# Performance work log

Hardware: AMD Instinct MI355X
Metric: run time of the kernel (lower is better)

Reference implementation:

```python
import jax, jax.numpy as jnp
import numpy as np

B, T, I, H = 64, 128, 1024, 4096
NNZ_IH, NNZ_HH = 262144, 1048576
LN_EPS = 1e-5


def spmm(rows, cols, vals, x, n_out):
    # y[r, b] = sum_{e: rows[e]==r} vals[e] * x[cols[e], b]
    return jax.ops.segment_sum(vals[:, None] * x[cols], rows, num_segments=n_out)


def setup_inputs() -> dict:
    key = jax.random.key(0)
    ks = jax.random.split(key, 8)
    x = jax.random.normal(ks[0], (B, T, I), dtype=jnp.float32)
    ih_rows = jax.random.randint(ks[1], (NNZ_IH,), 0, H, dtype=jnp.int32)
    ih_cols = jax.random.randint(ks[2], (NNZ_IH,), 0, I, dtype=jnp.int32)
    ih_vals = jax.random.normal(ks[3], (NNZ_IH,), dtype=jnp.float32) * 0.02
    hh_rows = jax.random.randint(ks[4], (NNZ_HH,), 0, H, dtype=jnp.int32)
    hh_cols = jax.random.randint(ks[5], (NNZ_HH,), 0, H, dtype=jnp.int32)
    hh_vals = jax.random.normal(ks[6], (NNZ_HH,), dtype=jnp.float32) * 0.02
    return {
        "x": x,
        "ih_rows": ih_rows, "ih_cols": ih_cols, "ih_vals": ih_vals,
        "hh_rows": hh_rows, "hh_cols": hh_cols, "hh_vals": hh_vals,
        "b_ih": jnp.zeros((H,), jnp.float32),
        "b_hh": jnp.zeros((H,), jnp.float32),
        "ln_gamma": jnp.ones((H,), jnp.float32),
        "ln_beta": jnp.zeros((H,), jnp.float32),
    }


def reference(x, ih_rows, ih_cols, ih_vals, hh_rows, hh_cols, hh_vals,
              b_ih, b_hh, ln_gamma, ln_beta):
    # batch_first input (B, T, I) -> (T, I, B), matching torch permute(1, 2, 0)
    xt = jnp.transpose(x, (1, 2, 0))

    def step(h, x_t):
        pre = (spmm(ih_rows, ih_cols, ih_vals, x_t, H) + b_ih[:, None]
               + spmm(hh_rows, hh_cols, hh_vals, h, H) + b_hh[:, None])
        h_act = jnp.tanh(pre)  # (H, B)
        # layernorm over hidden dim (applied on h.t() in torch)
        mu = jnp.mean(h_act, axis=0, keepdims=True)
        var = jnp.mean((h_act - mu) ** 2, axis=0, keepdims=True)
        h_norm = (h_act - mu) * jax.lax.rsqrt(var + LN_EPS)
        h_new = h_norm * ln_gamma[:, None] + ln_beta[:, None]
        return h_new, h_new

    h0 = jnp.zeros((H, B), jnp.float32)
    h_last, out = jax.lax.scan(step, h0, xt)  # out: (T, H, B)
    out = jnp.transpose(out, (2, 0, 1))       # (B, T, H) batch_first
    h_last = h_last.T                         # (B, H)
    return out, h_last
```

## Files before the change

kernel.cpp:

```cpp
#include <hip/hip_runtime.h>
#include <hip/hip_bf16.h>
#include <cstdint>

#define TT 128
#define BB 64
#define II 1024
#define HD 4096
#define N_IH 262144
#define N_HH 1048576
#define LN_EPS 1e-5f
#define NREP 16

typedef unsigned int u32;
typedef unsigned short u16;
typedef float f32x2 __attribute__((ext_vector_type(2)));

__device__ __forceinline__ u32 f2bf_bits(float f) {
  u32 u = __float_as_uint(f);
  return (u + 0x7FFFu + ((u >> 16) & 1u)) >> 16;
}


__global__ void k_hist(const int* __restrict__ rows, int n, int* __restrict__ hist) {
  int e = blockIdx.x * 256 + threadIdx.x;
  if (e < n) atomicAdd(&hist[rows[e] * 64 + (blockIdx.x & 63)], 1);
}

__global__ __launch_bounds__(256) void k_rowtot(const int* __restrict__ hist, int* __restrict__ rowtot) {
  int w = threadIdx.x >> 6, lane = threadIdx.x & 63;
  int row = blockIdx.x * 4 + w;
  int c = hist[row * 64 + lane];
#pragma unroll
  for (int d = 1; d < 64; d <<= 1) c += __shfl_xor(c, d);
  if (lane == 0) rowtot[row] = (c + 7) & ~7;
}

__global__ void k_scan2(const int* __restrict__ rowtot, int* __restrict__ rp) {
  int lane = threadIdx.x;
  int total = 0;
  for (int j = 0; j < 64; ++j) total += rowtot[lane * 64 + j];
  int x = total;
  for (int d = 1; d < 64; d <<= 1) {
    int y = __shfl_up(x, d, 64);
    if (lane >= d) x += y;
  }
  int run = x - total;
  for (int j = 0; j < 64; ++j) {
    int idx = lane * 64 + j;
    rp[idx] = run;
    run += rowtot[idx];
  }
  if (lane == 63) rp[HD] = run;
}

__global__ __launch_bounds__(256) void k_repbase(const int* __restrict__ hist, const int* __restrict__ rp,
                                                 int* __restrict__ cur) {
  int w = threadIdx.x >> 6, lane = threadIdx.x & 63;
  int row = blockIdx.x * 4 + w;
  int c = hist[row * 64 + lane];
  int x = c;
#pragma unroll
  for (int d = 1; d < 64; d <<= 1) {
    int y = __shfl_up(x, d, 64);
    if (lane >= d) x += y;
  }
  cur[row * 64 + lane] = rp[row] + (x - c);
}

__global__ void k_scatter(const int* __restrict__ rows, const int* __restrict__ cols,
                          const float* __restrict__ vals, int n,
                          int* __restrict__ cur, u32* __restrict__ meta,
                          const float* __restrict__ gamma, const float* __restrict__ beta,
                          float* __restrict__ rvg_rep, float* __restrict__ rvb_rep, int fold) {
  int e = blockIdx.x * 256 + threadIdx.x;
  if (e >= n) return;
  int rep = blockIdx.x & 63;
  int r = rows[e], c = cols[e];
  float v = vals[e];
  float vg = v;
  if (fold) {
    vg = v * gamma[c];
    atomicAdd(&rvg_rep[r * 64 + rep], vg);
    atomicAdd(&rvb_rep[r * 64 + rep], v * beta[c]);
  }
  u32 word = (f2bf_bits(vg) << 16) | (u32)c;
  int pos = atomicAdd(&cur[r * 64 + rep], 1);
  meta[pos] = word;
}

__global__ __launch_bounds__(256) void k_rvred(const float* __restrict__ rvg_rep,
                                               const float* __restrict__ rvb_rep,
                                               float* __restrict__ rowvg, float* __restrict__ rowvb) {
  int w = threadIdx.x >> 6, lane = threadIdx.x & 63;
  int row = blockIdx.x * 4 + w;
  float a = rvg_rep[row * 64 + lane];
  float b = rvb_rep[row * 64 + lane];
#pragma unroll
  for (int d = 1; d < 64; d <<= 1) { a += __shfl_xor(a, d); b += __shfl_xor(b, d); }
  if (lane == 0) { rowvg[row] = a; rowvb[row] = b; }
}

__global__ __launch_bounds__(256) void k_xt(const float* __restrict__ x, u16* __restrict__ xt) {
  __shared__ u16 tile[64][66];
  int t = blockIdx.x >> 4, i0 = (blockIdx.x & 15) << 6;
  int w = threadIdx.x >> 6, lane = threadIdx.x & 63;
#pragma unroll
  for (int k = 0; k < 16; ++k) {
    int b = w * 16 + k;
    float v = x[((size_t)b * TT + t) * II + i0 + lane];
    tile[b][lane] = (u16)f2bf_bits(v);
  }
  __syncthreads();
#pragma unroll
  for (int k = 0; k < 16; ++k) {
    int i = w * 16 + k;
    xt[((size_t)t * II + i0 + i) * BB + lane] = tile[lane][i];
  }
}


__device__ __forceinline__ uint4 gld(const char* base, u32 m) {
  return *(const uint4*)(base + ((int)(m & 0xFFFFu) << 7));
}

__device__ __forceinline__ void consume(u32 m, uint4 g, f32x2 acc[4]) {
  float vgf = __uint_as_float(m & 0xFFFF0000u);
  f32x2 vg2 = {vgf, vgf};
  f32x2 p0 = {__uint_as_float(g.x << 16), __uint_as_float(g.x & 0xFFFF0000u)};
  f32x2 p1 = {__uint_as_float(g.y << 16), __uint_as_float(g.y & 0xFFFF0000u)};
  f32x2 p2 = {__uint_as_float(g.z << 16), __uint_as_float(g.z & 0xFFFF0000u)};
  f32x2 p3 = {__uint_as_float(g.w << 16), __uint_as_float(g.w & 0xFFFF0000u)};
  acc[0] += vg2 * p0;
  acc[1] += vg2 * p1;
  acc[2] += vg2 * p2;
  acc[3] += vg2 * p3;
}

__device__ __forceinline__ void gather6(const u32* __restrict__ mp, int n,
                                        const char* __restrict__ base, f32x2 acc[4]) {
  if (n <= 0) return;
  u32 m0 = mp[0], m1 = mp[8], m2 = mp[16], m3 = mp[24], m4 = mp[32], m5 = mp[40];
  uint4 g0 = gld(base, m0), g1 = gld(base, m1), g2 = gld(base, m2),
        g3 = gld(base, m3), g4 = gld(base, m4);
#pragma unroll 6
  for (int it = 0; it < n; ++it) {
    u32 m6 = mp[(it + 6) * 8];
    uint4 g5 = gld(base, m5);
    consume(m0, g0, acc);
    m0 = m1; m1 = m2; m2 = m3; m3 = m4; m4 = m5; m5 = m6;
    g0 = g1; g1 = g2; g2 = g3; g3 = g4; g4 = g5;
  }
}

__global__ __launch_bounds__(256, 8) void k_step(
    const u32* __restrict__ meta_ih, const int* __restrict__ rp_ih,
    const u32* __restrict__ meta_hh, const int* __restrict__ rp_hh,
    const u16* __restrict__ xt_t, const u16* __restrict__ Aprev,
    u16* __restrict__ Acur,
    const float* __restrict__ st_prev, float* __restrict__ st_cur,
    const float* __restrict__ b_ih, const float* __restrict__ b_hh,
    const float* __restrict__ rowvg, const float* __restrict__ rowvb, int first) {
  __shared__ float s_mu[64], s_rs[64], s_sum[64], s_sq[64];
  __shared__ float epil[4][2][64];
  int tid = threadIdx.x;
  int w = tid >> 6, lane = tid & 63;
  if (tid < 64) { s_sum[tid] = 0.f; s_sq[tid] = 0.f; }
  if (!first && tid >= 64 && tid < 128) {
    int b = tid - 64;
    float s = 0.f, q = 0.f;
#pragma unroll
    for (int r2 = 0; r2 < NREP; ++r2) {
      s += st_prev[r2 * 64 + b];
      q += st_prev[NREP * 64 + r2 * 64 + b];
    }
    float mu = s * (1.0f / HD);
    float var = q * (1.0f / HD) - mu * mu;
    s_mu[b] = mu;
    s_rs[b] = rsqrtf(var + LN_EPS);
  }

  int row = blockIdx.x * 2 + (w >> 1);
  int half = w & 1;
  int grp = lane >> 3;
  int l = lane & 7;

  f32x2 acc[4] = {{0,0},{0,0},{0,0},{0,0}};
  {
    int s0 = rp_ih[row];
    int n = (rp_ih[row + 1] - s0) >> 3;
    int nA = (n + 1) >> 1;
    int nn = half ? (n - nA) : nA;
    int sb = s0 + (half ? nA * 8 : 0);
    gather6(meta_ih + sb + grp, nn, (const char*)xt_t + l * 16, acc);
  }
#pragma unroll
  for (int j = 0; j < 4; ++j) {
#pragma unroll
    for (int d = 8; d < 64; d <<= 1) {
      acc[j].x += __shfl_xor(acc[j].x, d);
      acc[j].y += __shfl_xor(acc[j].y, d);
    }
  }
  if (lane < 8) {
#pragma unroll
    for (int j = 0; j < 4; ++j) {
      epil[w][0][lane * 8 + 2 * j] = acc[j].x;
      epil[w][0][lane * 8 + 2 * j + 1] = acc[j].y;
    }
  }

#pragma unroll
  for (int j = 0; j < 4; ++j) { acc[j].x = 0.f; acc[j].y = 0.f; }
  if (!first) {
    int s0 = rp_hh[row];
    int n = (rp_hh[row + 1] - s0) >> 3;
    int nA = (n + 1) >> 1;
    int nn = half ? (n - nA) : nA;
    int sb = s0 + (half ? nA * 8 : 0);
    gather6(meta_hh + sb + grp, nn, (const char*)Aprev + l * 16, acc);
  }
#pragma unroll
  for (int j = 0; j < 4; ++j) {
#pragma unroll
    for (int d = 8; d < 64; d <<= 1) {
      acc[j].x += __shfl_xor(acc[j].x, d);
      acc[j].y += __shfl_xor(acc[j].y, d);
    }
  }
  if (lane < 8) {
#pragma unroll
    for (int j = 0; j < 4; ++j) {
      epil[w][1][lane * 8 + 2 * j] = acc[j].x;
      epil[w][1][lane * 8 + 2 * j + 1] = acc[j].y;
    }
  }

  __syncthreads();
  if (tid < 128) {
    int ridx = tid >> 6;
    int b = tid & 63;
    int row_e = blockIdx.x * 2 + ridx;
    float S_ih = epil[ridx * 2][0][b] + epil[ridx * 2 + 1][0][b];
    float bih = b_ih[row_e], bhh = b_hh[row_e];
    float pre;
    if (first) {
      pre = S_ih + bih + bhh;
    } else {
      float S_hh = epil[ridx * 2][1][b] + epil[ridx * 2 + 1][1][b];
      pre = S_ih + s_rs[b] * (S_hh - s_mu[b] * rowvg[row_e]) + (bih + bhh + rowvb[row_e]);
    }
    float h = 1.0f - 2.0f / (__expf(2.0f * pre) + 1.0f);
    Acur[(size_t)row_e * BB + b] = (u16)f2bf_bits(h);
    atomicAdd(&s_sum[b], h);
    atomicAdd(&s_sq[b], h * h);
  }
  __syncthreads();
  if (tid < 64) {
    int rep = blockIdx.x & (NREP - 1);
    atomicAdd(&st_cur[rep * 64 + tid], s_sum[tid]);
    atomicAdd(&st_cur[NREP * 64 + rep * 64 + tid], s_sq[tid]);
  }
}


__global__ __launch_bounds__(256) void k_out(const u16* __restrict__ A,
                                             const float* __restrict__ stats,
                                             const float* __restrict__ gamma,
                                             const float* __restrict__ beta,
                                             float* __restrict__ out) {
  __shared__ float s_mu[64], s_rs[64];
  __shared__ float tile[64][65];
  int t = blockIdx.x >> 6, r0 = (blockIdx.x & 63) << 6;
  int tid = threadIdx.x, w = tid >> 6, lane = tid & 63;
  const float* st = stats + (size_t)t * (2 * NREP * 64);
  if (tid < 64) {
    float s = 0.f, q = 0.f;
#pragma unroll
    for (int r2 = 0; r2 < NREP; ++r2) {
      s += st[r2 * 64 + tid];
      q += st[NREP * 64 + r2 * 64 + tid];
    }
    float mu = s * (1.0f / HD);
    float var = q * (1.0f / HD) - mu * mu;
    s_mu[tid] = mu;
    s_rs[tid] = rsqrtf(var + LN_EPS);
  }
  __syncthreads();
#pragma unroll
  for (int k = 0; k < 16; ++k) {
    int r = r0 + w * 16 + k;
    float a = __uint_as_float(((u32)A[((size_t)t * HD + r) * BB + lane]) << 16);
    float hn = (a - s_mu[lane]) * s_rs[lane] * gamma[r] + beta[r];
    tile[w * 16 + k][lane] = hn;
  }
  __syncthreads();
#pragma unroll
  for (int k = 0; k < 16; ++k) {
    int b = w * 16 + k;
    float v = tile[lane][b];
    out[((size_t)b * TT + t) * HD + r0 + lane] = v;
    if (t == TT - 1) out[(size_t)BB * TT * HD + (size_t)b * HD + r0 + lane] = v;
  }
}


extern "C" void kernel_launch(void* const* d_in, const int* in_sizes, int n_in,
                              void* d_out, int out_size, void* d_ws, size_t ws_size,
                              hipStream_t stream) {
  const float* x = (const float*)d_in[0];
  const int* ih_rows = (const int*)d_in[1];
  const int* ih_cols = (const int*)d_in[2];
  const float* ih_vals = (const float*)d_in[3];
  const int* hh_rows = (const int*)d_in[4];
  const int* hh_cols = (const int*)d_in[5];
  const float* hh_vals = (const float*)d_in[6];
  const float* b_ih = (const float*)d_in[7];
  const float* b_hh = (const float*)d_in[8];
  const float* gamma = (const float*)d_in[9];
  const float* beta = (const float*)d_in[10];

  char* ws = (char*)d_ws;
  u16* xt = (u16*)(ws + 0);
  u16* A = (u16*)(ws + 16777216);
  u32* meta_ih = (u32*)(ws + 83886080);
  u32* meta_hh = (u32*)(ws + 85065984);
  float* stats = (float*)(ws + 89391616);
  float* rowvg = (float*)(ws + 90440192);
  float* rowvb = (float*)(ws + 90456576);
  int* rp_ih = (int*)(ws + 90472960);
  int* rp_hh = (int*)(ws + 90489600);

  char* scr = ws + 50331648;
  int* hist_ih = (int*)(scr + 0);
  int* hist_hh = (int*)(scr + 1048576);
  int* cur_ih = (int*)(scr + 2097152);
  int* cur_hh = (int*)(scr + 3145728);
  float* rvg_rep = (float*)(scr + 4194304);
  float* rvb_rep = (float*)(scr + 5242880);
  int* rowtot_ih = (int*)(scr + 6291456);
  int* rowtot_hh = (int*)(scr + 6307840);

  hipMemsetAsync(scr, 0, 6291456, stream);
  hipMemsetAsync(ws + 83886080, 0, 6554112, stream);

  k_hist<<<N_IH / 256, 256, 0, stream>>>(ih_rows, N_IH, hist_ih);
  k_hist<<<N_HH / 256, 256, 0, stream>>>(hh_rows, N_HH, hist_hh);
  k_rowtot<<<HD / 4, 256, 0, stream>>>(hist_ih, rowtot_ih);
  k_rowtot<<<HD / 4, 256, 0, stream>>>(hist_hh, rowtot_hh);
  k_scan2<<<1, 64, 0, stream>>>(rowtot_ih, rp_ih);
  k_scan2<<<1, 64, 0, stream>>>(rowtot_hh, rp_hh);
  k_repbase<<<HD / 4, 256, 0, stream>>>(hist_ih, rp_ih, cur_ih);
  k_repbase<<<HD / 4, 256, 0, stream>>>(hist_hh, rp_hh, cur_hh);
  k_scatter<<<N_IH / 256, 256, 0, stream>>>(ih_rows, ih_cols, ih_vals, N_IH, cur_ih, meta_ih,
                                            gamma, beta, rvg_rep, rvb_rep, 0);
  k_scatter<<<N_HH / 256, 256, 0, stream>>>(hh_rows, hh_cols, hh_vals, N_HH, cur_hh, meta_hh,
                                            gamma, beta, rvg_rep, rvb_rep, 1);
  k_rvred<<<HD / 4, 256, 0, stream>>>(rvg_rep, rvb_rep, rowvg, rowvb);
  k_xt<<<TT * (II / 64), 256, 0, stream>>>(x, xt);

  for (int t = 0; t < TT; ++t) {
    const u16* xt_t = xt + (size_t)t * II * BB;
    const u16* Aprev = (t == 0) ? A : A + (size_t)(t - 1) * HD * BB;
    u16* Acur = A + (size_t)t * HD * BB;
    const float* st_prev = (t == 0) ? stats : stats + (size_t)(t - 1) * (2 * NREP * 64);
    float* st_cur = stats + (size_t)t * (2 * NREP * 64);
    k_step<<<HD / 2, 256, 0, stream>>>(meta_ih, rp_ih, meta_hh, rp_hh, xt_t, Aprev, Acur,
                                       st_prev, st_cur, b_ih, b_hh, rowvg, rowvb,
                                       (t == 0) ? 1 : 0);
  }

  k_out<<<TT * (HD / 64), 256, 0, stream>>>(A, stats, gamma, beta, (float*)d_out);
}
```

Before: 2.491 ms.

## Stage per-row sparse metadata in LDS before gathering, shorten prefetch depth

At the start of each step kernel, warps cooperatively copy the packed ih/hh metadata for the block's two rows into shared memory, in fixed-size chunks, while the last warp computes the layernorm statistics. The gather loop then reads metadata from LDS instead of global memory, and its in-flight gather depth drops from five to four with a smaller unroll. This removes dependent global metadata loads from the inner gather loop, at the cost of an extra barrier and a fixed-size copy that assumes each row's metadata fits within 768 (hh) and 256 (ih) entries, presumably guaranteed by padding done in the unseen setup code.

```diff
diff --git a/kernel.cpp b/kernel.cpp
--- a/kernel.cpp
+++ b/kernel.cpp
@@ -136,19 +136,18 @@
   acc[3] += vg2 * p3;
 }
 
-__device__ __forceinline__ void gather6(const u32* __restrict__ mp, int n,
+__device__ __forceinline__ void gatherL(const u32* __restrict__ lm, int n,
                                         const char* __restrict__ base, f32x2 acc[4]) {
   if (n <= 0) return;
-  u32 m0 = mp[0], m1 = mp[8], m2 = mp[16], m3 = mp[24], m4 = mp[32], m5 = mp[40];
-  uint4 g0 = gld(base, m0), g1 = gld(base, m1), g2 = gld(base, m2),
-        g3 = gld(base, m3), g4 = gld(base, m4);
-#pragma unroll 6
+  u32 m0 = lm[0], m1 = lm[8], m2 = lm[16], m3 = lm[24], m4 = lm[32], m5 = lm[40];
+  uint4 g0 = gld(base, m0), g1 = gld(base, m1), g2 = gld(base, m2), g3 = gld(base, m3);
+#pragma unroll 4
   for (int it = 0; it < n; ++it) {
-    u32 m6 = mp[(it + 6) * 8];
-    uint4 g5 = gld(base, m5);
+    u32 m6 = lm[(it + 6) * 8];
+    uint4 g4 = gld(base, m4);
     consume(m0, g0, acc);
     m0 = m1; m1 = m2; m2 = m3; m3 = m4; m4 = m5; m5 = m6;
-    g0 = g1; g1 = g2; g2 = g3; g3 = g4; g4 = g5;
+    g0 = g1; g1 = g2; g2 = g3; g3 = g4;
   }
 }
 
@@ -162,36 +161,56 @@
     const float* __restrict__ rowvg, const float* __restrict__ rowvb, int first) {
   __shared__ float s_mu[64], s_rs[64], s_sum[64], s_sq[64];
   __shared__ float epil[4][2][64];
+  __shared__ __align__(16) u32 lmeta_hh[2][768];
+  __shared__ __align__(16) u32 lmeta_ih[2][256];
   int tid = threadIdx.x;
   int w = tid >> 6, lane = tid & 63;
-  if (tid < 64) { s_sum[tid] = 0.f; s_sq[tid] = 0.f; }
-  if (!first && tid >= 64 && tid < 128) {
-    int b = tid - 64;
-    float s = 0.f, q = 0.f;
-#pragma unroll
-    for (int r2 = 0; r2 < NREP; ++r2) {
-      s += st_prev[r2 * 64 + b];
-      q += st_prev[NREP * 64 + r2 * 64 + b];
-    }
-    float mu = s * (1.0f / HD);
-    float var = q * (1.0f / HD) - mu * mu;
-    s_mu[b] = mu;
-    s_rs[b] = rsqrtf(var + LN_EPS);
-  }
-
-  int row = blockIdx.x * 2 + (w >> 1);
+  int r0 = blockIdx.x * 2;
+
+  if (w < 2) {
+    if (!first) {
+      int s0 = rp_hh[r0 + w];
+      const uint4* src = (const uint4*)(meta_hh + s0);
+      uint4* dst = (uint4*)(&lmeta_hh[w][0]);
+#pragma unroll
+      for (int k = 0; k < 3; ++k) dst[k * 64 + lane] = src[k * 64 + lane];
+    }
+  } else if (w == 2) {
+#pragma unroll
+    for (int i = 0; i < 2; ++i) {
+      int s0 = rp_ih[r0 + i];
+      ((uint4*)&lmeta_ih[i][0])[lane] = ((const uint4*)(meta_ih + s0))[lane];
+    }
+  } else {
+    s_sum[lane] = 0.f;
+    s_sq[lane] = 0.f;
+    if (!first) {
+      float s = 0.f, q = 0.f;
+#pragma unroll
+      for (int r2 = 0; r2 < NREP; ++r2) {
+        s += st_prev[r2 * 64 + lane];
+        q += st_prev[NREP * 64 + r2 * 64 + lane];
+      }
+      float mu = s * (1.0f / HD);
+      float var = q * (1.0f / HD) - mu * mu;
+      s_mu[lane] = mu;
+      s_rs[lane] = rsqrtf(var + LN_EPS);
+    }
+  }
+  __syncthreads();
+
+  int row = r0 + (w >> 1);
   int half = w & 1;
   int grp = lane >> 3;
   int l = lane & 7;
 
   f32x2 acc[4] = {{0,0},{0,0},{0,0},{0,0}};
   {
-    int s0 = rp_ih[row];
-    int n = (rp_ih[row + 1] - s0) >> 3;
+    int n = (rp_ih[row + 1] - rp_ih[row]) >> 3;
     int nA = (n + 1) >> 1;
     int nn = half ? (n - nA) : nA;
-    int sb = s0 + (half ? nA * 8 : 0);
-    gather6(meta_ih + sb + grp, nn, (const char*)xt_t + l * 16, acc);
+    const u32* lm = &lmeta_ih[w >> 1][(half ? nA * 8 : 0) + grp];
+    gatherL(lm, nn, (const char*)xt_t + l * 16, acc);
   }
 #pragma unroll
   for (int j = 0; j < 4; ++j) {
@@ -212,12 +231,11 @@
 #pragma unroll
   for (int j = 0; j < 4; ++j) { acc[j].x = 0.f; acc[j].y = 0.f; }
   if (!first) {
-    int s0 = rp_hh[row];
-    int n = (rp_hh[row + 1] - s0) >> 3;
+    int n = (rp_hh[row + 1] - rp_hh[row]) >> 3;
     int nA = (n + 1) >> 1;
     int nn = half ? (n - nA) : nA;
-    int sb = s0 + (half ? nA * 8 : 0);
-    gather6(meta_hh + sb + grp, nn, (const char*)Aprev + l * 16, acc);
+    const u32* lm = &lmeta_hh[w >> 1][(half ? nA * 8 : 0) + grp];
+    gatherL(lm, nn, (const char*)Aprev + l * 16, acc);
   }
 #pragma unroll
   for (int j = 0; j < 4; ++j) {
@@ -239,7 +257,7 @@
   if (tid < 128) {
     int ridx = tid >> 6;
     int b = tid & 63;
-    int row_e = blockIdx.x * 2 + ridx;
+    int row_e = r0 + ridx;
     float S_ih = epil[ridx * 2][0][b] + epil[ridx * 2 + 1][0][b];
     float bih = b_ih[row_e], bhh = b_hh[row_e];
     float pre;
```

New measurement: 2.330 ms. -6.5%, faster.
